# Kernel optimization log

Hardware: AMD Instinct MI355X
Metric: run time of the kernel (lower is better)

Reference implementation:

```python
import jax, jax.numpy as jnp
import numpy as np

GRID_RES = 64
BOUND = 1.2

def _coords():
    lin = jnp.linspace(-BOUND, BOUND, GRID_RES, dtype=jnp.float32)
    gx, gy, gz = jnp.meshgrid(lin, lin, lin, indexing='ij')
    return jnp.stack([gx, gy, gz], axis=-1).reshape(-1, 3)  # (R^3, 3)

def setup_inputs() -> dict:
    key = jax.random.key(0)
    ks = jax.random.split(key, 9)
    B, D, H = 2, 512, 512
    s_in = 1.0 / np.sqrt(D + 3)
    s_h = 1.0 / np.sqrt(H)
    return {
        'cad_latent': jax.random.normal(ks[0], (B, D), jnp.float32),
        'W0': jax.random.normal(ks[1], (D + 3, H), jnp.float32) * s_in,
        'b0': jax.random.normal(ks[2], (H,), jnp.float32) * s_in,
        'W1': jax.random.normal(ks[3], (H, H), jnp.float32) * s_h,
        'b1': jax.random.normal(ks[4], (H,), jnp.float32) * s_h,
        'W2': jax.random.normal(ks[5], (H, H), jnp.float32) * s_h,
        'b2': jax.random.normal(ks[6], (H,), jnp.float32) * s_h,
        'W3': jax.random.normal(ks[7], (H, 1), jnp.float32) * s_h,
        'b3': jax.random.normal(ks[8], (1,), jnp.float32) * s_h,
    }

def reference(cad_latent, W0, b0, W1, b1, W2, b2, W3, b3):
    B, D = cad_latent.shape
    coords = _coords()  # (P, 3), P = R^3
    # First layer: concat([latent, coords]) @ W0 decomposed to avoid
    # materializing the broadcast-concatenated (B, P, D+3) tensor.
    lat_part = cad_latent @ W0[:D]          # (B, H)
    coord_part = coords @ W0[D:]            # (P, H)
    h = jax.nn.silu(lat_part[:, None, :] + coord_part[None, :, :] + b0)  # (B, P, H)
    h = jax.nn.silu(h @ W1 + b1)
    h = jax.nn.silu(h @ W2 + b2)
    sdf = h @ W3 + b3                       # (B, P, 1)
    return sdf.reshape(B, GRID_RES, GRID_RES, GRID_RES)
```

## Files before the change

kernel.cpp:

```cpp
#include <hip/hip_runtime.h>

#define H 512
#define MTILE 64
#define NBLK 8192
#define STEPC (2.4f / 63.0f)

typedef _Float16 half8 __attribute__((ext_vector_type(8)));
typedef _Float16 half4_t __attribute__((ext_vector_type(4)));
typedef float floatx16 __attribute__((ext_vector_type(16)));
typedef float floatx4 __attribute__((ext_vector_type(4)));
typedef float floatx2 __attribute__((ext_vector_type(2)));

__device__ inline float silu_f(float x) {
    return __fdividef(x, 1.0f + __expf(-x));
}

__global__ void prep_latw(const float* __restrict__ lat, const float* __restrict__ W0,
                          const float* __restrict__ b0, float* __restrict__ latw) {
    __shared__ float sl[H];
    const int b = blockIdx.x;
    const int j = threadIdx.x;
    sl[j] = lat[b * H + j];
    __syncthreads();
    float acc = b0[j];
#pragma unroll 8
    for (int d = 0; d < H; ++d) acc += sl[d] * W0[d * H + j];
    latw[b * H + j] = acc;
}

__global__ void prep_w16(const float* __restrict__ W1, const float* __restrict__ W2,
                         _Float16* __restrict__ ws) {
    const int id = blockIdx.x * 512 + threadIdx.x;
    const int l = id >> 18;
    const int rem = id & 0x3FFFF;
    const int k = rem >> 9, n = rem & 511;
    const float w = (l == 0 ? W1 : W2)[rem];
    ws[((size_t)(l * 64 + (k >> 3)) * 512 + n) * 8 + (k & 7)] = (_Float16)w;
}

__global__ __launch_bounds__(512, 4) void mesh_main(
    const float* __restrict__ W0, const float* __restrict__ b1,
    const float* __restrict__ b2, const float* __restrict__ W3,
    const float* __restrict__ b3, const float* __restrict__ latw,
    const _Float16* __restrict__ wsB, float* __restrict__ out) {

    __shared__ _Float16 hbuf2[4096 * 8];
    __shared__ float lwbuf[2 * H];
    __shared__ float partials[8][MTILE];

    const int tid = threadIdx.x;
    const int wave = tid >> 6, lane = tid & 63;
    const int lm = lane & 31, hi = lane >> 5;
    const int bi = blockIdx.x;
    const int b = bi >> 12;
    const int p0 = (bi & 4095) << 6;
    const float c0 = -1.2f + (float)(p0 >> 12) * STEPC;
    const float c1 = -1.2f + (float)((p0 >> 6) & 63) * STEPC;

    {
        const int j = tid;
        const float lwv = latw[b * H + j]
                        + c0 * W0[(H + 0) * H + j]
                        + c1 * W0[(H + 1) * H + j];
        floatx2 v;
        v[0] = lwv;
        v[1] = W0[(H + 2) * H + j];
        *(floatx2*)&lwbuf[2 * j] = v;
    }
    __syncthreads();

    {
        const float c2v = -1.2f + (float)lane * STEPC;
#pragma unroll
        for (int s = 0; s < 8; ++s) {
            const int g = wave * 8 + s;
            const floatx4* lp = (const floatx4*)&lwbuf[g * 16];
            half8 hv;
#pragma unroll
            for (int i = 0; i < 4; ++i) {
                const floatx4 pv = lp[i];
                hv[2 * i + 0] = (_Float16)silu_f(pv[0] + c2v * pv[1]);
                hv[2 * i + 1] = (_Float16)silu_f(pv[2] + c2v * pv[3]);
            }
            *(half8*)&hbuf2[(g * 64 + lane) * 8] = hv;
        }
    }

    const _Float16* hb = hbuf2 + hi * 512 + lm * 8;
    const _Float16* wsl = wsB + ((size_t)hi * 512 + wave * 64 + lm) * 8;

    floatx16 acc[2][2];

    auto zero_acc = [&]() {
#pragma unroll
        for (int mb = 0; mb < 2; ++mb)
#pragma unroll
            for (int nt = 0; nt < 2; ++nt)
#pragma unroll
                for (int r = 0; r < 16; ++r) acc[mb][nt][r] = 0.f;
    };

    auto loadW = [&](int l, int ks, half8 (&wf)[2]) {
        const _Float16* p = wsl + (size_t)(l * 32 + ks) * 8192;
        wf[0] = *(const half8*)(p);
        wf[1] = *(const half8*)(p + 256);
    };

    auto compute = [&](int ks, half8 (&wf)[2]) {
        half8 a[2];
        const _Float16* hp = hb + ks * 1024;
        a[0] = *(const half8*)(hp);
        a[1] = *(const half8*)(hp + 256);
#pragma unroll
        for (int nt = 0; nt < 2; ++nt)
#pragma unroll
            for (int mb = 0; mb < 2; ++mb)
                acc[mb][nt] = __builtin_amdgcn_mfma_f32_32x32x16_f16(wf[nt], a[mb], acc[mb][nt], 0, 0, 0);
    };

    auto run_gemm = [&](int l) {
        half8 Wb0[2], Wb1[2], Wb2[2], Wb3[2];
        loadW(l, 0, Wb0);
        loadW(l, 1, Wb1);
#pragma unroll 1
        for (int ks = 0; ks < 32; ks += 4) {
            loadW(l, (ks + 2) & 31, Wb2);
            compute(ks, Wb0);
            loadW(l, (ks + 3) & 31, Wb3);
            compute(ks + 1, Wb1);
            loadW(l, (ks + 4) & 31, Wb0);
            compute(ks + 2, Wb2);
            loadW(l, (ks + 5) & 31, Wb1);
            compute(ks + 3, Wb3);
        }
    };

    zero_acc();
    __syncthreads();
    run_gemm(0);
    __syncthreads();
    {
        _Float16* wb = hbuf2 + (wave * 8) * 512 + lm * 8 + hi * 4;
        floatx4 b1v[2][4];
#pragma unroll
        for (int nt = 0; nt < 2; ++nt)
#pragma unroll
            for (int g = 0; g < 4; ++g)
                b1v[nt][g] = *(const floatx4*)&b1[wave * 64 + nt * 32 + g * 8 + hi * 4];
#pragma unroll
        for (int mb = 0; mb < 2; ++mb)
#pragma unroll
            for (int nt = 0; nt < 2; ++nt)
#pragma unroll
                for (int g = 0; g < 4; ++g) {
                    half4_t hv;
#pragma unroll
                    for (int j = 0; j < 4; ++j)
                        hv[j] = (_Float16)silu_f(acc[mb][nt][g * 4 + j] + b1v[nt][g][j]);
                    *(half4_t*)(wb + (nt * 4 + g) * 512 + mb * 256) = hv;
                }
    }

    zero_acc();
    __syncthreads();
    run_gemm(1);

    {
        floatx4 b2v[2][4], w3v[2][4];
#pragma unroll
        for (int nt = 0; nt < 2; ++nt)
#pragma unroll
            for (int g = 0; g < 4; ++g) {
                const int n0 = wave * 64 + nt * 32 + g * 8 + hi * 4;
                b2v[nt][g] = *(const floatx4*)&b2[n0];
                w3v[nt][g] = *(const floatx4*)&W3[n0];
            }
#pragma unroll
        for (int mb = 0; mb < 2; ++mb) {
            float sum = 0.f;
#pragma unroll
            for (int nt = 0; nt < 2; ++nt)
#pragma unroll
                for (int g = 0; g < 4; ++g)
#pragma unroll
                    for (int j = 0; j < 4; ++j)
                        sum += silu_f(acc[mb][nt][g * 4 + j] + b2v[nt][g][j]) * w3v[nt][g][j];
            sum += __shfl_xor(sum, 32);
            if (hi == 0) partials[wave][mb * 32 + lm] = sum;
        }
    }
    __syncthreads();
    if (tid < MTILE) {
        float o = b3[0];
#pragma unroll
        for (int w = 0; w < 8; ++w) o += partials[w][tid];
        out[(size_t)bi * MTILE + tid] = o;
    }
}

extern "C" void kernel_launch(void* const* d_in, const int* in_sizes, int n_in,
                              void* d_out, int out_size, void* d_ws, size_t ws_size,
                              hipStream_t stream) {
    const float* lat = (const float*)d_in[0];
    const float* W0  = (const float*)d_in[1];
    const float* b0  = (const float*)d_in[2];
    const float* W1  = (const float*)d_in[3];
    const float* b1  = (const float*)d_in[4];
    const float* W2  = (const float*)d_in[5];
    const float* b2  = (const float*)d_in[6];
    const float* W3  = (const float*)d_in[7];
    const float* b3  = (const float*)d_in[8];
    float* out = (float*)d_out;

    float* latw = (float*)d_ws;
    _Float16* wsB = (_Float16*)((char*)d_ws + 4096);

    prep_latw<<<2, 512, 0, stream>>>(lat, W0, b0, latw);
    prep_w16<<<1024, 512, 0, stream>>>(W1, W2, wsB);
    mesh_main<<<NBLK, 512, 0, stream>>>(W0, b1, b2, W3, b3, latw, wsB, out);
}
```

Baseline: 835.8 us.

## Halve points per block and widen per-wave N tile to 128 columns

Each block now handles 32 points with 4 waves, and each wave computes a 32x128 output tile using four MFMA accumulators that share one A fragment. LDS use per block is halved and the grid doubles, aiming for more resident blocks and simpler A-operand reuse. In exchange, every block still streams the full weight matrices for half as many points, doubling weight traffic per point from cache.

```diff
diff --git a/kernel.cpp b/kernel.cpp
--- a/kernel.cpp
+++ b/kernel.cpp
@@ -1,8 +1,8 @@
 #include <hip/hip_runtime.h>
 
 #define H 512
-#define MTILE 64
-#define NBLK 8192
+#define MTILE 32
+#define NBLK 16384
 #define STEPC (2.4f / 63.0f)
 
 typedef _Float16 half8 __attribute__((ext_vector_type(8)));
@@ -38,27 +38,29 @@
     ws[((size_t)(l * 64 + (k >> 3)) * 512 + n) * 8 + (k & 7)] = (_Float16)w;
 }
 
-__global__ __launch_bounds__(512, 4) void mesh_main(
+__global__ __launch_bounds__(256, 4) void mesh_main(
     const float* __restrict__ W0, const float* __restrict__ b1,
     const float* __restrict__ b2, const float* __restrict__ W3,
     const float* __restrict__ b3, const float* __restrict__ latw,
     const _Float16* __restrict__ wsB, float* __restrict__ out) {
 
-    __shared__ _Float16 hbuf2[4096 * 8];
+    __shared__ _Float16 hbuf2[2048 * 8];
     __shared__ float lwbuf[2 * H];
-    __shared__ float partials[8][MTILE];
+    __shared__ float partials[4][MTILE];
 
     const int tid = threadIdx.x;
     const int wave = tid >> 6, lane = tid & 63;
     const int lm = lane & 31, hi = lane >> 5;
     const int bi = blockIdx.x;
-    const int b = bi >> 12;
-    const int p0 = (bi & 4095) << 6;
+    const int b = bi >> 13;
+    const int p0 = (bi & 8191) << 5;
     const float c0 = -1.2f + (float)(p0 >> 12) * STEPC;
     const float c1 = -1.2f + (float)((p0 >> 6) & 63) * STEPC;
+    const float z0 = -1.2f + (float)(p0 & 63) * STEPC;
 
-    {
-        const int j = tid;
+#pragma unroll
+    for (int it = 0; it < 2; ++it) {
+        const int j = tid + it * 256;
         const float lwv = latw[b * H + j]
                         + c0 * W0[(H + 0) * H + j]
                         + c1 * W0[(H + 1) * H + j];
@@ -70,10 +72,10 @@
     __syncthreads();
 
     {
-        const float c2v = -1.2f + (float)lane * STEPC;
+        const float c2v = z0 + (float)lm * STEPC;
 #pragma unroll
         for (int s = 0; s < 8; ++s) {
-            const int g = wave * 8 + s;
+            const int g = wave * 16 + hi * 8 + s;
             const floatx4* lp = (const floatx4*)&lwbuf[g * 16];
             half8 hv;
 #pragma unroll
@@ -82,57 +84,48 @@
                 hv[2 * i + 0] = (_Float16)silu_f(pv[0] + c2v * pv[1]);
                 hv[2 * i + 1] = (_Float16)silu_f(pv[2] + c2v * pv[3]);
             }
-            *(half8*)&hbuf2[(g * 64 + lane) * 8] = hv;
+            *(half8*)&hbuf2[(g * 32 + lm) * 8] = hv;
         }
     }
 
-    const _Float16* hb = hbuf2 + hi * 512 + lm * 8;
-    const _Float16* wsl = wsB + ((size_t)hi * 512 + wave * 64 + lm) * 8;
+    const _Float16* hb = hbuf2 + hi * 256 + lm * 8;
+    const _Float16* wsl = wsB + ((size_t)hi * 512 + wave * 128 + lm) * 8;
 
-    floatx16 acc[2][2];
+    floatx16 acc[4];
 
     auto zero_acc = [&]() {
 #pragma unroll
-        for (int mb = 0; mb < 2; ++mb)
+        for (int j = 0; j < 4; ++j)
 #pragma unroll
-            for (int nt = 0; nt < 2; ++nt)
-#pragma unroll
-                for (int r = 0; r < 16; ++r) acc[mb][nt][r] = 0.f;
+            for (int r = 0; r < 16; ++r) acc[j][r] = 0.f;
     };
 
-    auto loadW = [&](int l, int ks, half8 (&wf)[2]) {
+    auto loadW = [&](int l, int ks, half8 (&wf)[4]) {
         const _Float16* p = wsl + (size_t)(l * 32 + ks) * 8192;
-        wf[0] = *(const half8*)(p);
-        wf[1] = *(const half8*)(p + 256);
+#pragma unroll
+        for (int j = 0; j < 4; ++j)
+            wf[j] = *(const half8*)(p + j * 256);
     };
 
-    auto compute = [&](int ks, half8 (&wf)[2]) {
-        half8 a[2];
-        const _Float16* hp = hb + ks * 1024;
-        a[0] = *(const half8*)(hp);
-        a[1] = *(const half8*)(hp + 256);
+    auto compute = [&](half8 (&wf)[4], half8 a) {
 #pragma unroll
-        for (int nt = 0; nt < 2; ++nt)
-#pragma unroll
-            for (int mb = 0; mb < 2; ++mb)
-                acc[mb][nt] = __builtin_amdgcn_mfma_f32_32x32x16_f16(wf[nt], a[mb], acc[mb][nt], 0, 0, 0);
+        for (int j = 0; j < 4; ++j)
+            acc[j] = __builtin_amdgcn_mfma_f32_32x32x16_f16(wf[j], a, acc[j], 0, 0, 0);
     };
 
     auto run_gemm = [&](int l) {
-        half8 Wb0[2], Wb1[2], Wb2[2], Wb3[2];
-        loadW(l, 0, Wb0);
-        loadW(l, 1, Wb1);
+        half8 Wb0[4], Wb1[4], a0, a1;
+        loadW(l, 0, Wb0); a0 = *(const half8*)(hb + 0 * 512);
+        loadW(l, 1, Wb1); a1 = *(const half8*)(hb + 1 * 512);
 #pragma unroll 1
-        for (int ks = 0; ks < 32; ks += 4) {
-            loadW(l, (ks + 2) & 31, Wb2);
-            compute(ks, Wb0);
-            loadW(l, (ks + 3) & 31, Wb3);
-            compute(ks + 1, Wb1);
-            loadW(l, (ks + 4) & 31, Wb0);
-            compute(ks + 2, Wb2);
-            loadW(l, (ks + 5) & 31, Wb1);
-            compute(ks + 3, Wb3);
+        for (int ks = 0; ks < 30; ks += 2) {
+            compute(Wb0, a0);
+            loadW(l, ks + 2, Wb0); a0 = *(const half8*)(hb + (ks + 2) * 512);
+            compute(Wb1, a1);
+            loadW(l, ks + 3, Wb1); a1 = *(const half8*)(hb + (ks + 3) * 512);
         }
+        compute(Wb0, a0);
+        compute(Wb1, a1);
     };
 
     zero_acc();
@@ -140,25 +133,18 @@
     run_gemm(0);
     __syncthreads();
     {
-        _Float16* wb = hbuf2 + (wave * 8) * 512 + lm * 8 + hi * 4;
-        floatx4 b1v[2][4];
+        _Float16* wb = hbuf2 + lm * 8 + hi * 4;
 #pragma unroll
-        for (int nt = 0; nt < 2; ++nt)
+        for (int j = 0; j < 4; ++j)
 #pragma unroll
-            for (int g = 0; g < 4; ++g)
-                b1v[nt][g] = *(const floatx4*)&b1[wave * 64 + nt * 32 + g * 8 + hi * 4];
+            for (int g = 0; g < 4; ++g) {
+                const floatx4 b1v = *(const floatx4*)&b1[wave * 128 + j * 32 + g * 8 + hi * 4];
+                half4_t hv;
 #pragma unroll
-        for (int mb = 0; mb < 2; ++mb)
-#pragma unroll
-            for (int nt = 0; nt < 2; ++nt)
-#pragma unroll
-                for (int g = 0; g < 4; ++g) {
-                    half4_t hv;
-#pragma unroll
-                    for (int j = 0; j < 4; ++j)
-                        hv[j] = (_Float16)silu_f(acc[mb][nt][g * 4 + j] + b1v[nt][g][j]);
-                    *(half4_t*)(wb + (nt * 4 + g) * 512 + mb * 256) = hv;
-                }
+                for (int r = 0; r < 4; ++r)
+                    hv[r] = (_Float16)silu_f(acc[j][g * 4 + r] + b1v[r]);
+                *(half4_t*)(wb + (wave * 16 + j * 4 + g) * 256) = hv;
+            }
     }
 
     zero_acc();
@@ -166,34 +152,26 @@
     run_gemm(1);
 
     {
-        floatx4 b2v[2][4], w3v[2][4];
+        float sum = 0.f;
 #pragma unroll
-        for (int nt = 0; nt < 2; ++nt)
+        for (int j = 0; j < 4; ++j)
 #pragma unroll
             for (int g = 0; g < 4; ++g) {
-                const int n0 = wave * 64 + nt * 32 + g * 8 + hi * 4;
-                b2v[nt][g] = *(const floatx4*)&b2[n0];
-                w3v[nt][g] = *(const floatx4*)&W3[n0];
+                const int n0 = wave * 128 + j * 32 + g * 8 + hi * 4;
+                const floatx4 b2v = *(const floatx4*)&b2[n0];
+                const floatx4 w3v = *(const floatx4*)&W3[n0];
+#pragma unroll
+                for (int r = 0; r < 4; ++r)
+                    sum += silu_f(acc[j][g * 4 + r] + b2v[r]) * w3v[r];
             }
-#pragma unroll
-        for (int mb = 0; mb < 2; ++mb) {
-            float sum = 0.f;
-#pragma unroll
-            for (int nt = 0; nt < 2; ++nt)
-#pragma unroll
-                for (int g = 0; g < 4; ++g)
-#pragma unroll
-                    for (int j = 0; j < 4; ++j)
-                        sum += silu_f(acc[mb][nt][g * 4 + j] + b2v[nt][g][j]) * w3v[nt][g][j];
-            sum += __shfl_xor(sum, 32);
-            if (hi == 0) partials[wave][mb * 32 + lm] = sum;
-        }
+        sum += __shfl_xor(sum, 32);
+        if (hi == 0) partials[wave][lm] = sum;
     }
     __syncthreads();
     if (tid < MTILE) {
         float o = b3[0];
 #pragma unroll
-        for (int w = 0; w < 8; ++w) o += partials[w][tid];
+        for (int w = 0; w < 4; ++w) o += partials[w][tid];
         out[(size_t)bi * MTILE + tid] = o;
     }
 }
@@ -217,5 +195,5 @@
 
     prep_latw<<<2, 512, 0, stream>>>(lat, W0, b0, latw);
     prep_w16<<<1024, 512, 0, stream>>>(W1, W2, wsB);
-    mesh_main<<<NBLK, 512, 0, stream>>>(W0, b1, b2, W3, b3, latw, wsB, out);
+    mesh_main<<<NBLK, 256, 0, stream>>>(W0, b1, b2, W3, b3, latw, wsB, out);
 }
```

New measurement: 909.6 us. 8.8% more time.
